# Performance work log

Measured on AMD Instinct MI355X. Metric: run time of the kernel, lower is better.

The kernel has to match this reference:

```python
import jax, jax.numpy as jnp
import numpy as np

ALPHA = 0.25
GAMMA = 2.0
# all cost weights are 1.0 per init defaults

def box_cxcywh_to_xyxy(b):
    cx, cy, w, h = b[..., 0], b[..., 1], b[..., 2], b[..., 3]
    return jnp.stack([cx - 0.5 * w, cy - 0.5 * h, cx + 0.5 * w, cy + 0.5 * h], axis=-1)

def generalized_box_iou(b1, b2):
    # b1: [B,Q,4], b2: [B,T,4] in xyxy -> [B,Q,T]
    area1 = (b1[..., 2] - b1[..., 0]) * (b1[..., 3] - b1[..., 1])  # [B,Q]
    area2 = (b2[..., 2] - b2[..., 0]) * (b2[..., 3] - b2[..., 1])  # [B,T]
    lt = jnp.maximum(b1[:, :, None, :2], b2[:, None, :, :2])        # [B,Q,T,2]
    rb = jnp.minimum(b1[:, :, None, 2:], b2[:, None, :, 2:])
    wh = jnp.clip(rb - lt, 0.0)
    inter = wh[..., 0] * wh[..., 1]
    union = area1[:, :, None] + area2[:, None, :] - inter
    iou = inter / union
    lt_c = jnp.minimum(b1[:, :, None, :2], b2[:, None, :, :2])
    rb_c = jnp.maximum(b1[:, :, None, 2:], b2[:, None, :, 2:])
    wh_c = jnp.clip(rb_c - lt_c, 0.0)
    area_c = wh_c[..., 0] * wh_c[..., 1]
    return iou - (area_c - union) / area_c

def point_sample_bilinear(img, pts):
    # img: [B,N,H,W]; pts: [P,2] (x,y) in [0,1]. Matches F.grid_sample
    # bilinear, align_corners=False, padding_mode='zeros'.
    H, W = img.shape[-2], img.shape[-1]
    x = pts[:, 0] * W - 0.5
    y = pts[:, 1] * H - 0.5
    x0 = jnp.floor(x); y0 = jnp.floor(y)
    wx1 = x - x0; wx0 = 1.0 - wx1
    wy1 = y - y0; wy0 = 1.0 - wy1

    def gather(yi, xi):
        valid = ((xi >= 0) & (xi < W) & (yi >= 0) & (yi < H)).astype(img.dtype)
        xc = jnp.clip(xi, 0, W - 1).astype(jnp.int32)
        yc = jnp.clip(yi, 0, H - 1).astype(jnp.int32)
        return img[:, :, yc, xc] * valid  # [B,N,P]

    return (gather(y0, x0) * (wy0 * wx0)
            + gather(y0, x0 + 1) * (wy0 * wx1)
            + gather(y0 + 1, x0) * (wy1 * wx0)
            + gather(y0 + 1, x0 + 1) * (wy1 * wx1))

def point_sample_nearest(img, pts):
    # grid_sample nearest, align_corners=False, zeros padding
    H, W = img.shape[-2], img.shape[-1]
    x = jnp.round(pts[:, 0] * W - 0.5)
    y = jnp.round(pts[:, 1] * H - 0.5)
    valid = ((x >= 0) & (x < W) & (y >= 0) & (y < H)).astype(img.dtype)
    xc = jnp.clip(x, 0, W - 1).astype(jnp.int32)
    yc = jnp.clip(y, 0, H - 1).astype(jnp.int32)
    return img[:, :, yc, xc] * valid  # [B,N,P]

def setup_inputs() -> dict:
    key = jax.random.key(0)
    ks = jax.random.split(key, 7)
    B, Q, C, T, H, W = 2, 900, 91, 64, 128, 128
    P = H * W // 16  # mask_point_sample_ratio = 16
    return {
        "pred_logits": jax.random.normal(ks[0], (B, Q, C), jnp.float32),
        "pred_boxes": jax.random.uniform(ks[1], (B, Q, 4), jnp.float32),
        "pred_masks": jax.random.normal(ks[2], (B, Q, H, W), jnp.float32),
        "tgt_boxes": jax.random.uniform(ks[3], (B, T, 4), jnp.float32),
        "tgt_masks": jax.random.uniform(ks[4], (B, T, H, W), jnp.float32),
        "point_coords": jax.random.uniform(ks[5], (1, P, 2), jnp.float32),
        "tgt_labels": jax.random.randint(ks[6], (B, T), 0, C, jnp.int32),
    }

def reference(pred_logits, pred_boxes, pred_masks, tgt_boxes, tgt_masks, point_coords, tgt_labels):
    # ---- focal classification cost ----
    prob = jax.nn.sigmoid(pred_logits)                          # [B,Q,C]
    neg_cost = (1 - ALPHA) * prob ** GAMMA * (-jax.nn.log_sigmoid(-pred_logits))
    pos_cost = ALPHA * (1 - prob) ** GAMMA * (-jax.nn.log_sigmoid(pred_logits))
    diff = pos_cost - neg_cost                                   # [B,Q,C]
    cost_class = jnp.take_along_axis(diff, tgt_labels[:, None, :], axis=2)  # [B,Q,T]

    # ---- L1 bbox cost (cdist p=1) ----
    cost_bbox = jnp.abs(pred_boxes[:, :, None, :] - tgt_boxes[:, None, :, :]).sum(-1)

    # ---- GIoU cost ----
    giou = generalized_box_iou(box_cxcywh_to_xyxy(pred_boxes), box_cxcywh_to_xyxy(tgt_boxes))

    # ---- point-sampled mask CE / Dice costs ----
    pts = point_coords[0]                                        # [P,2]
    P = pts.shape[0]
    pred_pts = point_sample_bilinear(pred_masks, pts)            # [B,Q,P]
    tgt_pts = point_sample_nearest(tgt_masks, pts)               # [B,T,P]
    pos_ce = -jax.nn.log_sigmoid(pred_pts)
    neg_ce = -jax.nn.log_sigmoid(-pred_pts)
    cost_ce = (jnp.einsum('bqp,btp->bqt', pos_ce, tgt_pts)
               + jnp.einsum('bqp,btp->bqt', neg_ce, 1.0 - tgt_pts)) / P
    s = jax.nn.sigmoid(pred_pts)
    numer = 2.0 * jnp.einsum('bqp,btp->bqt', s, tgt_pts)
    denom = s.sum(-1)[:, :, None] + tgt_pts.sum(-1)[:, None, :]
    cost_dice = 1.0 - (numer + 1.0) / (denom + 1.0)

    C = (cost_bbox + cost_class - giou + cost_ce + cost_dice).astype(jnp.float32)
    # replace non-finite entries by 2 * (per-batch max finite cost)
    fin = jnp.isfinite(C)
    max_cost = jnp.max(jnp.where(fin, C, 0.0), axis=(1, 2), keepdims=True)
    C = jnp.where(fin, C, 2.0 * max_cost)
    return C
```

## Files before the change

kernel.cpp:

```cpp
#include <hip/hip_runtime.h>
#include <hip/hip_bf16.h>
#include <math.h>

#define B_    2
#define Q_    900
#define QPAD_ 912
#define MT_   57
#define CC_   91
#define T_    64
#define H_    128
#define W_    128
#define HW_   (H_*W_)
#define P_    1024
#define FLT_BIG 3.402823466e+38f

typedef short short8 __attribute__((ext_vector_type(8)));
typedef float f32x4  __attribute__((ext_vector_type(4)));

static __device__ __forceinline__ unsigned short f2bf(float v) {
    __hip_bfloat16 h = __float2bfloat16(v);
    return *reinterpret_cast<unsigned short*>(&h);
}

__global__ __launch_bounds__(256) void kS_sample(
    const float* __restrict__ tgt_masks,
    const float* __restrict__ pred_masks,
    const float* __restrict__ pc,
    unsigned short* __restrict__ tgtPT,
    float* __restrict__ tsum,
    unsigned short* __restrict__ xsbuf,
    float* __restrict__ lneg,
    float* __restrict__ lsum,
    float* __restrict__ bmax)
{
    const int tid = threadIdx.x;
    const int wv = tid >> 6, lane = tid & 63;
    __shared__ float sSum[2][4];

    if (blockIdx.x < B_*T_) {
        if (blockIdx.x == 0 && tid < B_) bmax[tid] = 0.f;
        const int bt = blockIdx.x;
        const float* __restrict__ img = tgt_masks + (size_t)bt * HW_;

        float vals[4];
        #pragma unroll
        for (int k = 0; k < 4; ++k) {
            int p = tid*4 + k;
            float px = pc[2*p], py = pc[2*p+1];
            float xf = rintf(px * (float)W_ - 0.5f);
            float yf = rintf(py * (float)H_ - 0.5f);
            bool nv = (xf >= 0.f) && (xf < (float)W_) && (yf >= 0.f) && (yf < (float)H_);
            int xc = (int)fminf(fmaxf(xf, 0.f), (float)(W_-1));
            int yc = (int)fminf(fmaxf(yf, 0.f), (float)(H_-1));
            vals[k] = nv ? img[yc*W_ + xc] : 0.f;
        }
        *(ushort4*)(tgtPT + (size_t)bt*P_ + tid*4) =
            make_ushort4(f2bf(vals[0]), f2bf(vals[1]), f2bf(vals[2]), f2bf(vals[3]));

        float local = (vals[0] + vals[1]) + (vals[2] + vals[3]);
        #pragma unroll
        for (int off = 32; off; off >>= 1) local += __shfl_down(local, off);
        if (lane == 0) sSum[0][wv] = local;
        __syncthreads();
        if (tid == 0) tsum[bt] = (sSum[0][0]+sSum[0][1]) + (sSum[0][2]+sSum[0][3]);
    } else {
        const int bq = blockIdx.x - B_*T_;
        const int b = bq / Q_, q = bq % Q_;
        const float* __restrict__ img = pred_masks + (size_t)bq * HW_;

        int   o[4][4];
        float ww[4][4];
        #pragma unroll
        for (int k = 0; k < 4; ++k) {
            int p = tid*4 + k;
            float px = pc[2*p], py = pc[2*p+1];
            float x = px * (float)W_ - 0.5f;
            float y = py * (float)H_ - 0.5f;
            float x0f = floorf(x), y0f = floorf(y);
            float wx1 = x - x0f, wy1 = y - y0f;
            float wx0 = 1.f - wx1, wy0 = 1.f - wy1;
            int x0 = (int)x0f, y0 = (int)y0f;
            int   xs2[2] = {x0, x0+1}, ys2[2] = {y0, y0+1};
            float wxs[2] = {wx0, wx1}, wys[2] = {wy0, wy1};
            #pragma unroll
            for (int dy = 0; dy < 2; ++dy)
            #pragma unroll
            for (int dx = 0; dx < 2; ++dx) {
                int xi = xs2[dx], yi = ys2[dy];
                bool v = (xi >= 0) && (xi < W_) && (yi >= 0) && (yi < H_);
                int xcc = min(max(xi, 0), W_-1);
                int ycc = min(max(yi, 0), H_-1);
                o [k][dy*2+dx] = ycc*W_ + xcc;
                ww[k][dy*2+dx] = v ? wys[dy]*wxs[dx] : 0.f;
            }
        }

        float tap[4][4];
        #pragma unroll
        for (int k = 0; k < 4; ++k) {
            tap[k][0] = img[o[k][0]]; tap[k][1] = img[o[k][1]];
            tap[k][2] = img[o[k][2]]; tap[k][3] = img[o[k][3]];
        }

        float ln = 0.f, ls = 0.f;
        unsigned short px[4], ps[4];
        #pragma unroll
        for (int k = 0; k < 4; ++k) {
            float x = ww[k][0]*tap[k][0] + ww[k][1]*tap[k][1]
                    + ww[k][2]*tap[k][2] + ww[k][3]*tap[k][3];
            float e  = __expf(-fabsf(x));
            float sp = __logf(1.f + e) + fmaxf(x, 0.f);
            float r  = 1.f / (1.f + e);
            float s  = (x >= 0.f) ? r : e * r;
            ln += sp; ls += s;
            px[k] = f2bf(x); ps[k] = f2bf(s);
        }

        *(ushort4*)(xsbuf + ((size_t)(b*2+0)*QPAD_ + q)*P_ + tid*4) = make_ushort4(px[0],px[1],px[2],px[3]);
        *(ushort4*)(xsbuf + ((size_t)(b*2+1)*QPAD_ + q)*P_ + tid*4) = make_ushort4(ps[0],ps[1],ps[2],ps[3]);

        #pragma unroll
        for (int off = 32; off; off >>= 1) {
            ln += __shfl_down(ln, off);
            ls += __shfl_down(ls, off);
        }
        if (lane == 0) { sSum[0][wv] = ln; sSum[1][wv] = ls; }
        __syncthreads();
        if (tid == 0) {
            lneg[b*Q_ + q] = (sSum[0][0]+sSum[0][1]) + (sSum[0][2]+sSum[0][3]);
            lsum[b*Q_ + q] = (sSum[1][0]+sSum[1][1]) + (sSum[1][2]+sSum[1][3]);
        }
    }
}

__global__ __launch_bounds__(256) void k3_gemm(
    const unsigned short* __restrict__ xsbuf,
    const unsigned short* __restrict__ tgtPT,
    const float* __restrict__ lneg,
    const float* __restrict__ lsum,
    const float* __restrict__ tsum,
    const float* __restrict__ pred_logits,
    const float* __restrict__ pred_boxes,
    const float* __restrict__ tgt_boxes,
    const int*   __restrict__ tgt_labels,
    float* __restrict__ out,
    float* __restrict__ bmax)
{
    __shared__ f32x4 sAcc[4][64][8];

    const int bid = blockIdx.x;
    const int b = bid / MT_, mt = bid % MT_;
    const int w = threadIdx.x >> 6, l = threadIdx.x & 63;
    const int ml = l & 15, kg = l >> 4;

    const short* Ax = (const short*)xsbuf + ((size_t)(b*2+0)*QPAD_ + mt*16 + ml)*P_ + kg*8 + w*256;
    const short* As = (const short*)xsbuf + ((size_t)(b*2+1)*QPAD_ + mt*16 + ml)*P_ + kg*8 + w*256;
    const short* Bb = (const short*)tgtPT + ((size_t)(b*T_) + ml)*P_ + kg*8 + w*256;

    f32x4 accX[4] = {{0,0,0,0},{0,0,0,0},{0,0,0,0},{0,0,0,0}};
    f32x4 accS[4] = {{0,0,0,0},{0,0,0,0},{0,0,0,0},{0,0,0,0}};

    #pragma unroll
    for (int kt = 0; kt < 8; ++kt) {
        const int ko = kt * 32;
        short8 afx = *(const short8*)(Ax + ko);
        short8 afs = *(const short8*)(As + ko);
        #pragma unroll
        for (int nt = 0; nt < 4; ++nt) {
            short8 bf = *(const short8*)(Bb + (size_t)nt*16*P_ + ko);
            accX[nt] = __builtin_amdgcn_mfma_f32_16x16x32_bf16(afx, bf, accX[nt], 0, 0, 0);
            accS[nt] = __builtin_amdgcn_mfma_f32_16x16x32_bf16(afs, bf, accS[nt], 0, 0, 0);
        }
    }

    #pragma unroll
    for (int nt = 0; nt < 4; ++nt) {
        sAcc[w][l][nt*2+0] = accX[nt];
        sAcc[w][l][nt*2+1] = accS[nt];
    }
    __syncthreads();

    f32x4 aX = sAcc[0][l][w*2+0];
    f32x4 aS = sAcc[0][l][w*2+1];
    #pragma unroll
    for (int w2 = 1; w2 < 4; ++w2) {
        aX += sAcc[w2][l][w*2+0];
        aS += sAcc[w2][l][w*2+1];
    }

    const int t = w*16 + ml;
    const float tsu = tsum[b*T_ + t];
    const int   lab = tgt_labels[b*T_ + t];
    const float4 tbx = *(const float4*)(tgt_boxes + (size_t)(b*T_ + t)*4);
    float tx1 = tbx.x - 0.5f*tbx.z, ty1 = tbx.y - 0.5f*tbx.w;
    float tx2 = tbx.x + 0.5f*tbx.z, ty2 = tbx.y + 0.5f*tbx.w;
    float a2 = (tx2-tx1)*(ty2-ty1);

    float mloc = 0.f;

    #pragma unroll
    for (int r = 0; r < 4; ++r) {
        int q = mt*16 + kg*4 + r;
        int qc = min(q, Q_-1);
        float ln  = lneg[b*Q_ + qc];
        float lsv = lsum[b*Q_ + qc];
        float4 pb = *(const float4*)(pred_boxes + (size_t)(b*Q_ + qc)*4);
        float lg = pred_logits[((size_t)(b*Q_ + qc))*CC_ + lab];

        float ce   = (ln - aX[r]) * (1.f/(float)P_);
        float dice = 1.f - (2.f*aS[r] + 1.f) / (lsv + tsu + 1.f);

        float e  = __expf(-fabsf(lg));
        float lp = log1pf(e);
        float sp_neg = lp + fmaxf(-lg, 0.f);
        float sp_pos = lp + fmaxf( lg, 0.f);
        float prob = 1.f / (1.f + __expf(-lg));
        float cclass = 0.25f*(1.f-prob)*(1.f-prob)*sp_neg - 0.75f*prob*prob*sp_pos;

        float cbbox = fabsf(pb.x-tbx.x) + fabsf(pb.y-tbx.y) + fabsf(pb.z-tbx.z) + fabsf(pb.w-tbx.w);
        float px1 = pb.x - 0.5f*pb.z, py1 = pb.y - 0.5f*pb.w;
        float px2 = pb.x + 0.5f*pb.z, py2 = pb.y + 0.5f*pb.w;
        float a1 = (px2-px1)*(py2-py1);
        float iw = fmaxf(fminf(px2,tx2) - fmaxf(px1,tx1), 0.f);
        float ih = fmaxf(fminf(py2,ty2) - fmaxf(py1,ty1), 0.f);
        float inter = iw*ih;
        float uni = a1 + a2 - inter;
        float iou = inter / uni;
        float cw = fmaxf(fmaxf(px2,tx2) - fminf(px1,tx1), 0.f);
        float ch = fmaxf(fmaxf(py2,ty2) - fminf(py1,ty1), 0.f);
        float ac = cw*ch;
        float giou = iou - (ac - uni)/ac;

        float cost = cbbox + cclass - giou + ce + dice;
        if (q < Q_) {
            out[((size_t)(b*Q_ + q))*T_ + t] = cost;
            float cand = (fabsf(cost) <= FLT_BIG) ? cost : 0.f;
            mloc = fmaxf(mloc, cand);
        }
    }

    #pragma unroll
    for (int off = 32; off; off >>= 1) mloc = fmaxf(mloc, __shfl_down(mloc, off));
    __shared__ float sm[4];
    if (l == 0) sm[w] = mloc;
    __syncthreads();
    if (threadIdx.x == 0) {
        float bm = fmaxf(fmaxf(sm[0], sm[1]), fmaxf(sm[2], sm[3]));
        atomicMax((unsigned int*)&bmax[b], __float_as_uint(bm));
    }
}

__global__ __launch_bounds__(256) void k5_fix(float* __restrict__ out,
                                              const float* __restrict__ bmax)
{
    int i = blockIdx.x*256 + threadIdx.x;
    if (i >= B_*Q_*T_) return;
    float v = out[i];
    if (!(fabsf(v) <= FLT_BIG))
        out[i] = 2.f * bmax[i / (Q_*T_)];
}

extern "C" void kernel_launch(void* const* d_in, const int* in_sizes, int n_in,
                              void* d_out, int out_size, void* d_ws, size_t ws_size,
                              hipStream_t stream) {
    const float* pred_logits  = (const float*)d_in[0];
    const float* pred_boxes   = (const float*)d_in[1];
    const float* pred_masks   = (const float*)d_in[2];
    const float* tgt_boxes    = (const float*)d_in[3];
    const float* tgt_masks    = (const float*)d_in[4];
    const float* point_coords = (const float*)d_in[5];
    const int*   tgt_labels   = (const int*)d_in[6];
    float* out = (float*)d_out;

    char* w = (char*)d_ws;
    unsigned short* tgtPT = (unsigned short*)w;
    unsigned short* xsbuf = (unsigned short*)(w + 262144);
    size_t xs_bytes = (size_t)B_*2*QPAD_*P_*2;
    char* w2 = w + 262144 + xs_bytes;
    float* tsum = (float*)w2;
    float* lneg = (float*)(w2 + 512);
    float* lsum = (float*)(w2 + 512 + 7296);
    float* bmax = (float*)(w2 + 512 + 2*7296);

    kS_sample<<<B_*T_ + B_*Q_, 256, 0, stream>>>(tgt_masks, pred_masks, point_coords,
                                                 tgtPT, tsum, xsbuf, lneg, lsum, bmax);
    k3_gemm<<<B_*MT_, 256, 0, stream>>>(xsbuf, tgtPT, lneg, lsum, tsum,
                                        pred_logits, pred_boxes, tgt_boxes, tgt_labels, out, bmax);
    k5_fix<<<(B_*Q_*T_ + 255)/256, 256, 0, stream>>>(out, bmax);
}
```

Baseline: 47.83 us.

## Split GEMM tiles across target columns and pair bilinear taps into float2 loads

The GEMM kernel now launches four times as many blocks, each handling a single 16-target column tile instead of all four. This spreads 114 blocks' worth of work over 456 blocks to fill the GPU better, and the epilogue becomes one output per thread with a transposed shared reduction. In the sampling kernel, the bilinear gather clamps x to W-2 and loads two adjacent pixels per row with one 8-byte load, remapping weights at the edges. The cost is extra redundant A-tile loads from global memory across the column blocks and more atomics on bmax.

```diff
diff --git a/kernel.cpp b/kernel.cpp
--- a/kernel.cpp
+++ b/kernel.cpp
@@ -68,56 +68,52 @@
         const int b = bq / Q_, q = bq % Q_;
         const float* __restrict__ img = pred_masks + (size_t)bq * HW_;
 
-        int   o[4][4];
-        float ww[4][4];
+        int   base0[4], base1[4];
+        float wp0[4], wp1[4], wyv0[4], wyv1[4];
         #pragma unroll
         for (int k = 0; k < 4; ++k) {
             int p = tid*4 + k;
             float px = pc[2*p], py = pc[2*p+1];
-            float x = px * (float)W_ - 0.5f;
-            float y = py * (float)H_ - 0.5f;
-            float x0f = floorf(x), y0f = floorf(y);
-            float wx1 = x - x0f, wy1 = y - y0f;
-            float wx0 = 1.f - wx1, wy0 = 1.f - wy1;
+            float xf = px * (float)W_ - 0.5f;
+            float yf = py * (float)H_ - 0.5f;
+            float x0f = floorf(xf), y0f = floorf(yf);
+            float wx1 = xf - x0f, wx0 = 1.f - wx1;
+            float wy1 = yf - y0f, wy0 = 1.f - wy1;
             int x0 = (int)x0f, y0 = (int)y0f;
-            int   xs2[2] = {x0, x0+1}, ys2[2] = {y0, y0+1};
-            float wxs[2] = {wx0, wx1}, wys[2] = {wy0, wy1};
-            #pragma unroll
-            for (int dy = 0; dy < 2; ++dy)
-            #pragma unroll
-            for (int dx = 0; dx < 2; ++dx) {
-                int xi = xs2[dx], yi = ys2[dy];
-                bool v = (xi >= 0) && (xi < W_) && (yi >= 0) && (yi < H_);
-                int xcc = min(max(xi, 0), W_-1);
-                int ycc = min(max(yi, 0), H_-1);
-                o [k][dy*2+dx] = ycc*W_ + xcc;
-                ww[k][dy*2+dx] = v ? wys[dy]*wxs[dx] : 0.f;
-            }
-        }
-
-        float tap[4][4];
-        #pragma unroll
-        for (int k = 0; k < 4; ++k) {
-            tap[k][0] = img[o[k][0]]; tap[k][1] = img[o[k][1]];
-            tap[k][2] = img[o[k][2]]; tap[k][3] = img[o[k][3]];
+            int xa = min(max(x0, 0), W_-2);
+            wp0[k] = (x0 == xa) ? wx0 : ((x0 < xa) ? wx1 : 0.f);
+            wp1[k] = (x0 == xa) ? wx1 : ((x0 > xa) ? wx0 : 0.f);
+            wyv0[k] = (y0 >= 0 && y0 < H_)       ? wy0 : 0.f;
+            wyv1[k] = (y0+1 >= 0 && y0+1 < H_)   ? wy1 : 0.f;
+            int ya0 = min(max(y0,   0), H_-1);
+            int ya1 = min(max(y0+1, 0), H_-1);
+            base0[k] = ya0*W_ + xa;
+            base1[k] = ya1*W_ + xa;
+        }
+
+        float2 r0[4], r1[4];
+        #pragma unroll
+        for (int k = 0; k < 4; ++k) {
+            __builtin_memcpy(&r0[k], img + base0[k], 8);
+            __builtin_memcpy(&r1[k], img + base1[k], 8);
         }
 
         float ln = 0.f, ls = 0.f;
-        unsigned short px[4], ps[4];
-        #pragma unroll
-        for (int k = 0; k < 4; ++k) {
-            float x = ww[k][0]*tap[k][0] + ww[k][1]*tap[k][1]
-                    + ww[k][2]*tap[k][2] + ww[k][3]*tap[k][3];
+        unsigned short px_[4], ps_[4];
+        #pragma unroll
+        for (int k = 0; k < 4; ++k) {
+            float x = wyv0[k]*(wp0[k]*r0[k].x + wp1[k]*r0[k].y)
+                    + wyv1[k]*(wp0[k]*r1[k].x + wp1[k]*r1[k].y);
             float e  = __expf(-fabsf(x));
             float sp = __logf(1.f + e) + fmaxf(x, 0.f);
-            float r  = 1.f / (1.f + e);
-            float s  = (x >= 0.f) ? r : e * r;
+            float rr = 1.f / (1.f + e);
+            float s  = (x >= 0.f) ? rr : e * rr;
             ln += sp; ls += s;
-            px[k] = f2bf(x); ps[k] = f2bf(s);
-        }
-
-        *(ushort4*)(xsbuf + ((size_t)(b*2+0)*QPAD_ + q)*P_ + tid*4) = make_ushort4(px[0],px[1],px[2],px[3]);
-        *(ushort4*)(xsbuf + ((size_t)(b*2+1)*QPAD_ + q)*P_ + tid*4) = make_ushort4(ps[0],ps[1],ps[2],ps[3]);
+            px_[k] = f2bf(x); ps_[k] = f2bf(s);
+        }
+
+        *(ushort4*)(xsbuf + ((size_t)(b*2+0)*QPAD_ + q)*P_ + tid*4) = make_ushort4(px_[0],px_[1],px_[2],px_[3]);
+        *(ushort4*)(xsbuf + ((size_t)(b*2+1)*QPAD_ + q)*P_ + tid*4) = make_ushort4(ps_[0],ps_[1],ps_[2],ps_[3]);
 
         #pragma unroll
         for (int off = 32; off; off >>= 1) {
@@ -146,97 +142,91 @@
     float* __restrict__ out,
     float* __restrict__ bmax)
 {
-    __shared__ f32x4 sAcc[4][64][8];
+    __shared__ float sT[2][4][4][65];
 
     const int bid = blockIdx.x;
-    const int b = bid / MT_, mt = bid % MT_;
+    const int b = bid / (MT_*4);
+    const int rem = bid % (MT_*4);
+    const int mt = rem >> 2, nt = rem & 3;
     const int w = threadIdx.x >> 6, l = threadIdx.x & 63;
     const int ml = l & 15, kg = l >> 4;
 
     const short* Ax = (const short*)xsbuf + ((size_t)(b*2+0)*QPAD_ + mt*16 + ml)*P_ + kg*8 + w*256;
     const short* As = (const short*)xsbuf + ((size_t)(b*2+1)*QPAD_ + mt*16 + ml)*P_ + kg*8 + w*256;
-    const short* Bb = (const short*)tgtPT + ((size_t)(b*T_) + ml)*P_ + kg*8 + w*256;
-
-    f32x4 accX[4] = {{0,0,0,0},{0,0,0,0},{0,0,0,0},{0,0,0,0}};
-    f32x4 accS[4] = {{0,0,0,0},{0,0,0,0},{0,0,0,0},{0,0,0,0}};
+    const short* Bb = (const short*)tgtPT + ((size_t)(b*T_) + nt*16 + ml)*P_ + kg*8 + w*256;
+
+    f32x4 accX = {0,0,0,0};
+    f32x4 accS = {0,0,0,0};
 
     #pragma unroll
     for (int kt = 0; kt < 8; ++kt) {
         const int ko = kt * 32;
         short8 afx = *(const short8*)(Ax + ko);
         short8 afs = *(const short8*)(As + ko);
-        #pragma unroll
-        for (int nt = 0; nt < 4; ++nt) {
-            short8 bf = *(const short8*)(Bb + (size_t)nt*16*P_ + ko);
-            accX[nt] = __builtin_amdgcn_mfma_f32_16x16x32_bf16(afx, bf, accX[nt], 0, 0, 0);
-            accS[nt] = __builtin_amdgcn_mfma_f32_16x16x32_bf16(afs, bf, accS[nt], 0, 0, 0);
-        }
+        short8 bf  = *(const short8*)(Bb + ko);
+        accX = __builtin_amdgcn_mfma_f32_16x16x32_bf16(afx, bf, accX, 0, 0, 0);
+        accS = __builtin_amdgcn_mfma_f32_16x16x32_bf16(afs, bf, accS, 0, 0, 0);
     }
 
     #pragma unroll
-    for (int nt = 0; nt < 4; ++nt) {
-        sAcc[w][l][nt*2+0] = accX[nt];
-        sAcc[w][l][nt*2+1] = accS[nt];
+    for (int r = 0; r < 4; ++r) {
+        sT[0][r][w][l] = accX[r];
+        sT[1][r][w][l] = accS[r];
     }
     __syncthreads();
 
-    f32x4 aX = sAcc[0][l][w*2+0];
-    f32x4 aS = sAcc[0][l][w*2+1];
-    #pragma unroll
-    for (int w2 = 1; w2 < 4; ++w2) {
-        aX += sAcc[w2][l][w*2+0];
-        aS += sAcc[w2][l][w*2+1];
-    }
-
-    const int t = w*16 + ml;
+    const int tid = threadIdx.x;
+    const int ql = tid >> 4, tc = tid & 15;
+    const int r   = ql & 3;
+    const int src = (ql >> 2)*16 + tc;
+
+    float aX = ((sT[0][r][0][src] + sT[0][r][1][src]) + (sT[0][r][2][src] + sT[0][r][3][src]));
+    float aS = ((sT[1][r][0][src] + sT[1][r][1][src]) + (sT[1][r][2][src] + sT[1][r][3][src]));
+
+    const int q = mt*16 + ql;
+    const int t = nt*16 + tc;
+    const int qc = min(q, Q_-1);
+
     const float tsu = tsum[b*T_ + t];
     const int   lab = tgt_labels[b*T_ + t];
     const float4 tbx = *(const float4*)(tgt_boxes + (size_t)(b*T_ + t)*4);
+    float ln  = lneg[b*Q_ + qc];
+    float lsv = lsum[b*Q_ + qc];
+    float4 pb = *(const float4*)(pred_boxes + (size_t)(b*Q_ + qc)*4);
+    float lg  = pred_logits[((size_t)(b*Q_ + qc))*CC_ + lab];
+
+    float ce   = (ln - aX) * (1.f/(float)P_);
+    float dice = 1.f - (2.f*aS + 1.f) / (lsv + tsu + 1.f);
+
+    float e  = __expf(-fabsf(lg));
+    float lp = log1pf(e);
+    float sp_neg = lp + fmaxf(-lg, 0.f);
+    float sp_pos = lp + fmaxf( lg, 0.f);
+    float prob = 1.f / (1.f + __expf(-lg));
+    float cclass = 0.25f*(1.f-prob)*(1.f-prob)*sp_neg - 0.75f*prob*prob*sp_pos;
+
+    float cbbox = fabsf(pb.x-tbx.x) + fabsf(pb.y-tbx.y) + fabsf(pb.z-tbx.z) + fabsf(pb.w-tbx.w);
+    float px1 = pb.x - 0.5f*pb.z, py1 = pb.y - 0.5f*pb.w;
+    float px2 = pb.x + 0.5f*pb.z, py2 = pb.y + 0.5f*pb.w;
     float tx1 = tbx.x - 0.5f*tbx.z, ty1 = tbx.y - 0.5f*tbx.w;
     float tx2 = tbx.x + 0.5f*tbx.z, ty2 = tbx.y + 0.5f*tbx.w;
+    float a1 = (px2-px1)*(py2-py1);
     float a2 = (tx2-tx1)*(ty2-ty1);
-
+    float iw = fmaxf(fminf(px2,tx2) - fmaxf(px1,tx1), 0.f);
+    float ih = fmaxf(fminf(py2,ty2) - fmaxf(py1,ty1), 0.f);
+    float inter = iw*ih;
+    float uni = a1 + a2 - inter;
+    float iou = inter / uni;
+    float cw = fmaxf(fmaxf(px2,tx2) - fminf(px1,tx1), 0.f);
+    float ch = fmaxf(fmaxf(py2,ty2) - fminf(py1,ty1), 0.f);
+    float ac = cw*ch;
+    float giou = iou - (ac - uni)/ac;
+
+    float cost = cbbox + cclass - giou + ce + dice;
     float mloc = 0.f;
-
-    #pragma unroll
-    for (int r = 0; r < 4; ++r) {
-        int q = mt*16 + kg*4 + r;
-        int qc = min(q, Q_-1);
-        float ln  = lneg[b*Q_ + qc];
-        float lsv = lsum[b*Q_ + qc];
-        float4 pb = *(const float4*)(pred_boxes + (size_t)(b*Q_ + qc)*4);
-        float lg = pred_logits[((size_t)(b*Q_ + qc))*CC_ + lab];
-
-        float ce   = (ln - aX[r]) * (1.f/(float)P_);
-        float dice = 1.f - (2.f*aS[r] + 1.f) / (lsv + tsu + 1.f);
-
-        float e  = __expf(-fabsf(lg));
-        float lp = log1pf(e);
-        float sp_neg = lp + fmaxf(-lg, 0.f);
-        float sp_pos = lp + fmaxf( lg, 0.f);
-        float prob = 1.f / (1.f + __expf(-lg));
-        float cclass = 0.25f*(1.f-prob)*(1.f-prob)*sp_neg - 0.75f*prob*prob*sp_pos;
-
-        float cbbox = fabsf(pb.x-tbx.x) + fabsf(pb.y-tbx.y) + fabsf(pb.z-tbx.z) + fabsf(pb.w-tbx.w);
-        float px1 = pb.x - 0.5f*pb.z, py1 = pb.y - 0.5f*pb.w;
-        float px2 = pb.x + 0.5f*pb.z, py2 = pb.y + 0.5f*pb.w;
-        float a1 = (px2-px1)*(py2-py1);
-        float iw = fmaxf(fminf(px2,tx2) - fmaxf(px1,tx1), 0.f);
-        float ih = fmaxf(fminf(py2,ty2) - fmaxf(py1,ty1), 0.f);
-        float inter = iw*ih;
-        float uni = a1 + a2 - inter;
-        float iou = inter / uni;
-        float cw = fmaxf(fmaxf(px2,tx2) - fminf(px1,tx1), 0.f);
-        float ch = fmaxf(fmaxf(py2,ty2) - fminf(py1,ty1), 0.f);
-        float ac = cw*ch;
-        float giou = iou - (ac - uni)/ac;
-
-        float cost = cbbox + cclass - giou + ce + dice;
-        if (q < Q_) {
-            out[((size_t)(b*Q_ + q))*T_ + t] = cost;
-            float cand = (fabsf(cost) <= FLT_BIG) ? cost : 0.f;
-            mloc = fmaxf(mloc, cand);
-        }
+    if (q < Q_) {
+        out[((size_t)(b*Q_ + q))*T_ + t] = cost;
+        mloc = (fabsf(cost) <= FLT_BIG) ? fmaxf(cost, 0.f) : 0.f;
     }
 
     #pragma unroll
@@ -244,7 +234,7 @@
     __shared__ float sm[4];
     if (l == 0) sm[w] = mloc;
     __syncthreads();
-    if (threadIdx.x == 0) {
+    if (tid == 0) {
         float bm = fmaxf(fmaxf(sm[0], sm[1]), fmaxf(sm[2], sm[3]));
         atomicMax((unsigned int*)&bmax[b], __float_as_uint(bm));
     }
@@ -284,7 +274,7 @@
 
     kS_sample<<<B_*T_ + B_*Q_, 256, 0, stream>>>(tgt_masks, pred_masks, point_coords,
                                                  tgtPT, tsum, xsbuf, lneg, lsum, bmax);
-    k3_gemm<<<B_*MT_, 256, 0, stream>>>(xsbuf, tgtPT, lneg, lsum, tsum,
-                                        pred_logits, pred_boxes, tgt_boxes, tgt_labels, out, bmax);
+    k3_gemm<<<B_*MT_*4, 256, 0, stream>>>(xsbuf, tgtPT, lneg, lsum, tsum,
+                                          pred_logits, pred_boxes, tgt_boxes, tgt_labels, out, bmax);
     k5_fix<<<(B_*Q_*T_ + 255)/256, 256, 0, stream>>>(out, bmax);
 }
```

Result: no change. 47.63 us (-0.4%).
